# Kernel tuning notes

Hardware: AMD Instinct MI355X
Metric: run time of the kernel (lower is better)

Reference implementation:

```python
import jax, jax.numpy as jnp
import numpy as np

EMB = 512
HEADS = 8


def setup_inputs() -> dict:
    key = jax.random.key(0)
    ks = jax.random.split(key, 9)
    b, t, k, h = 4, 2048, EMB, HEADS
    s = 1.0 / np.sqrt(k)
    x = jax.random.normal(ks[0], (b, t, k), dtype=jnp.float32)
    Wq = jax.random.normal(ks[1], (k, h * k), dtype=jnp.float32) * s
    bq = jnp.zeros((h * k,), dtype=jnp.float32)
    Wk = jax.random.normal(ks[2], (k, h * k), dtype=jnp.float32) * s
    bk = jnp.zeros((h * k,), dtype=jnp.float32)
    Wv = jax.random.normal(ks[3], (k, h * k), dtype=jnp.float32) * s
    bv = jnp.zeros((h * k,), dtype=jnp.float32)
    Wo = jax.random.normal(ks[4], (h * k, k), dtype=jnp.float32) * (1.0 / np.sqrt(h * k))
    bo = jnp.zeros((k,), dtype=jnp.float32)
    return {"x": x, "Wq": Wq, "bq": bq, "Wk": Wk, "bk": bk,
            "Wv": Wv, "bv": bv, "Wo": Wo, "bo": bo}


def reference(x, Wq, bq, Wk, bk, Wv, bv, Wo, bo):
    b, t, k = x.shape
    h = Wq.shape[1] // k
    scale = k ** (-0.25)  # applied to both q and k, matching /= k**(1/4)
    # projections: [b,t,k] -> [b,t,h,k] -> [b,h,t,k]
    q = (x @ Wq + bq).reshape(b, t, h, k).transpose(0, 2, 1, 3) * scale
    kk = (x @ Wk + bk).reshape(b, t, h, k).transpose(0, 2, 1, 3) * scale
    v = (x @ Wv + bv).reshape(b, t, h, k).transpose(0, 2, 1, 3)
    # attention scores [b,h,t,t]
    scores = jnp.einsum('bhqk,bhsk->bhqs', q, kk)
    w = jax.nn.softmax(scores, axis=-1)
    out = jnp.einsum('bhqs,bhsk->bhqk', w, v)  # [b,h,t,k]
    out = out.transpose(0, 2, 1, 3).reshape(b, t, h * k)
    return out @ Wo + bo
```

## Files before the change

### kernel.cpp

```cpp
#include <hip/hip_runtime.h>
#include <hip/hip_bf16.h>
#include <stdint.h>

typedef __hip_bfloat16 bf16;
typedef __bf16 bf16x8 __attribute__((ext_vector_type(8)));
typedef float floatx4 __attribute__((ext_vector_type(4)));

#define AS_LDS __attribute__((address_space(3)))
#define AS_GLB __attribute__((address_space(1)))

__device__ __forceinline__ void gload_lds16(const bf16* g, bf16* l) {
    __builtin_amdgcn_global_load_lds((const AS_GLB void*)g, (AS_LDS void*)l, 16, 0, 0);
}

__global__ void probe_dtype(const float* __restrict__ x, int* __restrict__ flag) {
    __shared__ int cnt;
    if (threadIdx.x == 0) cnt = 0;
    __syncthreads();
    int ok = 0;
    for (int i = threadIdx.x; i < 4096; i += 256) {
        float v = x[i];
        if (v == v && fabsf(v) < 1.0e3f) ok++;
    }
    atomicAdd(&cnt, ok);
    __syncthreads();
    if (threadIdx.x == 0) *flag = (cnt > 2048) ? 1 : 0;
}

__global__ __launch_bounds__(256) void zero_f32(float* __restrict__ p, int n) {
    int i = blockIdx.x * 256 + threadIdx.x;
    if (i < n) p[i] = 0.f;
}

__global__ __launch_bounds__(256) void convert_to_bf16(
    const void* __restrict__ in, bf16* __restrict__ out, long n,
    const int* __restrict__ flag)
{
    long i = ((long)blockIdx.x * 256 + threadIdx.x) * 8;
    if (i >= n) return;
    bf16 o[8];
    if (*flag) {
        const float* p = (const float*)in + i;
        float4 a = *(const float4*)p;
        float4 b = *(const float4*)(p + 4);
        o[0] = __float2bfloat16(a.x); o[1] = __float2bfloat16(a.y);
        o[2] = __float2bfloat16(a.z); o[3] = __float2bfloat16(a.w);
        o[4] = __float2bfloat16(b.x); o[5] = __float2bfloat16(b.y);
        o[6] = __float2bfloat16(b.z); o[7] = __float2bfloat16(b.w);
    } else {
        *(float4*)o = *(const float4*)((const bf16*)in + i);
    }
    *(float4*)&out[i] = *(float4*)o;
}

__global__ __launch_bounds__(256) void emit_out(
    const bf16* __restrict__ in, void* __restrict__ out, long n,
    const int* __restrict__ flag)
{
    long i = ((long)blockIdx.x * 256 + threadIdx.x) * 8;
    if (i >= n) return;
    bf16 v[8];
    *(float4*)v = *(const float4*)&in[i];
    if (*flag) {
        float* o = (float*)out + i;
        float4 a, b;
        a.x = __bfloat162float(v[0]); a.y = __bfloat162float(v[1]);
        a.z = __bfloat162float(v[2]); a.w = __bfloat162float(v[3]);
        b.x = __bfloat162float(v[4]); b.y = __bfloat162float(v[5]);
        b.z = __bfloat162float(v[6]); b.w = __bfloat162float(v[7]);
        *(float4*)o = a;
        *(float4*)(o + 4) = b;
    } else {
        *(float4*)((bf16*)out + i) = *(float4*)v;
    }
}

__global__ __launch_bounds__(256) void transpose_any(
    const void* __restrict__ inv, bf16* __restrict__ out,
    int ldin, int ldout, const int* __restrict__ flag)
{
    __shared__ bf16 tile[64][80];
    const int fp32 = *flag;
    const int c0 = blockIdx.x * 64;
    const int r0 = blockIdx.y * 64;
    const int tid = threadIdx.x;
#pragma unroll
    for (int it = 0; it < 2; ++it) {
        int ch = tid + it * 256;
        int r = ch >> 3, c = (ch & 7) * 8;
        long eidx = (long)(r0 + r) * ldin + (c0 + c);
        if (fp32) {
            const float* p = (const float*)inv + eidx;
            float4 a = *(const float4*)p;
            float4 b = *(const float4*)(p + 4);
            bf16 o[8];
            o[0] = __float2bfloat16(a.x); o[1] = __float2bfloat16(a.y);
            o[2] = __float2bfloat16(a.z); o[3] = __float2bfloat16(a.w);
            o[4] = __float2bfloat16(b.x); o[5] = __float2bfloat16(b.y);
            o[6] = __float2bfloat16(b.z); o[7] = __float2bfloat16(b.w);
            *(float4*)&tile[r][c] = *(float4*)o;
        } else {
            *(float4*)&tile[r][c] = *(const float4*)((const bf16*)inv + eidx);
        }
    }
    __syncthreads();
#pragma unroll
    for (int it = 0; it < 2; ++it) {
        int ch = tid + it * 256;
        int oc = ch >> 3, rb = (ch & 7) * 8;
        bf16 tmp[8];
#pragma unroll
        for (int i = 0; i < 8; ++i) tmp[i] = tile[rb + i][oc];
        *(float4*)&out[(long)(c0 + oc) * ldout + r0 + rb] = *(float4*)tmp;
    }
}

__global__ __launch_bounds__(256) void transpose_bf16(
    const bf16* __restrict__ in, bf16* __restrict__ out,
    int ldin, int ldout,
    int nz1, long in_z1, long out_z1, long in_z2, long out_z2)
{
    __shared__ bf16 tile[64][80];
    const int z = blockIdx.z;
    const int z1 = z % nz1, z2 = z / nz1;
    in  += (long)z1 * in_z1 + (long)z2 * in_z2;
    out += (long)z1 * out_z1 + (long)z2 * out_z2;
    const int c0 = blockIdx.x * 64;
    const int r0 = blockIdx.y * 64;
    const int tid = threadIdx.x;
#pragma unroll
    for (int it = 0; it < 2; ++it) {
        int ch = tid + it * 256;
        int r = ch >> 3, c = (ch & 7) * 8;
        *(float4*)&tile[r][c] = *(const float4*)&in[(long)(r0 + r) * ldin + c0 + c];
    }
    __syncthreads();
#pragma unroll
    for (int it = 0; it < 2; ++it) {
        int ch = tid + it * 256;
        int oc = ch >> 3, rb = (ch & 7) * 8;
        bf16 tmp[8];
#pragma unroll
        for (int i = 0; i < 8; ++i) tmp[i] = tile[rb + i][oc];
        *(float4*)&out[(long)(c0 + oc) * ldout + r0 + rb] = *(float4*)tmp;
    }
}

template <int MODE, int SWZ>
__global__ __launch_bounds__(512, 2) void gemm256(
    const bf16* __restrict__ A, const bf16* __restrict__ Bt,
    bf16* __restrict__ C, const bf16* __restrict__ bias,
    int lda, int ldb, int ldc,
    long az, long bz, long cz, int K, float scale, int qcols,
    bf16* __restrict__ Vt, int vcol0, float* __restrict__ Lsum)
{
    __shared__ bf16 AsL[2][2][256 * 32];
    __shared__ bf16 BsL[2][2][256 * 32];

    const int tid  = threadIdx.x;
    const int lane = tid & 63;
    const int wave = tid >> 6;
    const int wr = wave >> 2;
    const int wc = wave & 3;
    const int lm = lane & 15;
    const int cl = lane >> 4;

    int bxx = blockIdx.x, byy = blockIdx.y, bzz = blockIdx.z;
    if constexpr (SWZ == 1) {
        int flat = bxx + (byy << 3) + (bzz << 6);
        int xcd = flat & 7, idx = flat >> 3;
        bzz = xcd; bxx = idx & 7; byy = idx >> 3;
    } else if constexpr (SWZ == 2) {
        int flat = bxx + byy * 48;
        int xcd = flat & 7, idx = flat >> 3;
        bxx = xcd * 6 + idx % 6; byy = idx / 6; bzz = 0;
    }
    const long zz = bzz;
    A  += zz * az;
    Bt += zz * bz;
    C  += zz * cz;
    float* Lz = (MODE == 1) ? (Lsum + zz * 2048) : nullptr;
    const int m0 = byy * 256;
    const int n0 = bxx * 256;

    int offA[8], offB[4];
#pragma unroll
    for (int i = 0; i < 8; ++i) {
        int row = wr * 128 + i * 16 + lm;
        offA[i] = row * 32 + ((cl ^ ((row >> 1) & 3)) << 3);
    }
#pragma unroll
    for (int j = 0; j < 4; ++j) {
        int row = wc * 64 + j * 16 + lm;
        offB[j] = row * 32 + ((cl ^ ((row >> 1) & 3)) << 3);
    }

    const int sr = lane >> 2;
    const int sc = lane & 3;
    const int NT = K >> 6;

    floatx4 acc[8][4];
#pragma unroll
    for (int i = 0; i < 8; ++i)
#pragma unroll
        for (int j = 0; j < 4; ++j)
            acc[i][j] = (floatx4){0.f, 0.f, 0.f, 0.f};

    auto stageU = [&](int which, int t, int kh) {
        if (t >= NT) return;
        const bf16* G = which ? Bt : A;
        const int ldg  = which ? ldb : lda;
        const int g0   = which ? n0 : m0;
        bf16* lb = which ? &BsL[t & 1][kh][0] : &AsL[t & 1][kh][0];
        const int kcol = t * 64 + kh * 32;
#pragma unroll
        for (int ii = 0; ii < 2; ++ii) {
            int row = ii * 128 + wave * 16 + sr;
            int cg  = sc ^ ((row >> 1) & 3);
            gload_lds16(G + (long)(g0 + row) * ldg + kcol + cg * 8,
                        lb + row * 32 + sc * 8);
        }
    };

    bf16x8 af[8], bfv[2];
    auto dsA = [&](int b, int kh) {
        const bf16* p = &AsL[b][kh][0];
#pragma unroll
        for (int i = 0; i < 8; ++i) af[i] = *(const bf16x8*)(p + offA[i]);
    };
    auto dsB = [&](int b, int kh, int nh) {
        const bf16* p = &BsL[b][kh][0];
        bfv[0] = *(const bf16x8*)(p + offB[nh * 2]);
        bfv[1] = *(const bf16x8*)(p + offB[nh * 2 + 1]);
    };
    auto mfmaQ = [&](int nh) {
        __builtin_amdgcn_s_setprio(1);
#pragma unroll
        for (int i = 0; i < 8; ++i) {
            acc[i][nh * 2] = __builtin_amdgcn_mfma_f32_16x16x32_bf16(
                af[i], bfv[0], acc[i][nh * 2], 0, 0, 0);
            acc[i][nh * 2 + 1] = __builtin_amdgcn_mfma_f32_16x16x32_bf16(
                af[i], bfv[1], acc[i][nh * 2 + 1], 0, 0, 0);
        }
        __builtin_amdgcn_s_setprio(0);
    };

#define BAR    __builtin_amdgcn_s_barrier()
#define SBZ    __builtin_amdgcn_sched_barrier(0)
#define LGKM0  do { asm volatile("s_waitcnt lgkmcnt(0)" ::: "memory"); SBZ; } while (0)
#define VM(n)  do { asm volatile("s_waitcnt vmcnt(" #n ")" ::: "memory"); SBZ; } while (0)

    stageU(0, 0, 0); stageU(1, 0, 0); stageU(0, 0, 1); stageU(1, 0, 1);
    stageU(0, 1, 0); stageU(1, 1, 0);
    VM(4);
    BAR;

    for (int t0 = 0; t0 < NT; t0 += 2) {
        const bool last = (t0 + 2 >= NT);
        dsA(0, 0); dsB(0, 0, 0); stageU(0, t0 + 1, 1);
        BAR; LGKM0; mfmaQ(0); BAR;
        dsB(0, 0, 1); stageU(1, t0 + 1, 1);
        BAR; LGKM0; mfmaQ(1); BAR;
        dsA(0, 1); dsB(0, 1, 0); stageU(0, t0 + 2, 0);
        BAR; LGKM0; mfmaQ(0); BAR;
        dsB(0, 1, 1); stageU(1, t0 + 2, 0);
        BAR; LGKM0; mfmaQ(1);
        if (last) { VM(0); } else { VM(4); }
        BAR;
        dsA(1, 0); dsB(1, 0, 0); stageU(0, t0 + 2, 1);
        BAR; LGKM0; mfmaQ(0); BAR;
        dsB(1, 0, 1); stageU(1, t0 + 2, 1);
        BAR; LGKM0; mfmaQ(1); BAR;
        dsA(1, 1); dsB(1, 1, 0); stageU(0, t0 + 3, 0);
        BAR; LGKM0; mfmaQ(0); BAR;
        dsB(1, 1, 1); stageU(1, t0 + 3, 0);
        BAR; LGKM0; mfmaQ(1);
        if (!last) { VM(4); }
        BAR;
    }
#undef BAR
#undef SBZ
#undef LGKM0
#undef VM

    const int cr = (lane >> 4) * 4;
    if constexpr (MODE == 1) {
#pragma unroll
        for (int j = 0; j < 4; ++j) {
            long q = n0 + wc * 64 + j * 16 + lm;
            bf16* Cr = C + q * ldc + m0 + wr * 128;
            float rs = 0.f;
#pragma unroll
            for (int i = 0; i < 8; ++i) {
                bf16 pk[4];
#pragma unroll
                for (int r = 0; r < 4; ++r) {
                    float e = __expf(acc[i][j][r]);
                    rs += e;
                    pk[r] = __float2bfloat16(e);
                }
                __builtin_nontemporal_store(*(const uint64_t*)pk,
                                            (uint64_t*)&Cr[i * 16 + cr]);
            }
            rs += __shfl_xor(rs, 16);
            rs += __shfl_xor(rs, 32);
            if (cl == 0) atomicAdd(&Lz[q], rs);
        }
    } else {
        if (n0 >= vcol0) {
#pragma unroll
            for (int j = 0; j < 4; ++j) {
                int col = n0 + wc * 64 + j * 16 + lm;
                float bv = __bfloat162float(bias[col]);
                int eg = col - vcol0;
                bf16* vt = Vt + ((long)(eg >> 9) * 512 + (eg & 511)) * 2048;
#pragma unroll
                for (int i = 0; i < 8; ++i) {
                    int t0v = m0 + wr * 128 + i * 16 + cr;
                    bf16 pk[4];
#pragma unroll
                    for (int r = 0; r < 4; ++r)
                        pk[r] = __float2bfloat16(acc[i][j][r] + bv);
                    *(uint64_t*)&vt[t0v] = *(const uint64_t*)pk;
                }
            }
        } else {
            const int l4 = lane & 3;
            float bvj[4], scj[4];
#pragma unroll
            for (int j = 0; j < 4; ++j) {
                int col = n0 + wc * 64 + j * 16 + lm;
                bvj[j] = __bfloat162float(bias[col]);
                scj[j] = (col < qcols) ? scale : 1.0f;
            }
#pragma unroll
            for (int i = 0; i < 8; ++i) {
                int row = m0 + wr * 128 + i * 16 + cr + l4;
                bf16* Cr = C + (long)row * ldc + n0 + wc * 64 + (lm & ~3);
#pragma unroll
                for (int j = 0; j < 4; ++j) {
                    float x0 = (acc[i][j][0] + bvj[j]) * scj[j];
                    float x1 = (acc[i][j][1] + bvj[j]) * scj[j];
                    float x2 = (acc[i][j][2] + bvj[j]) * scj[j];
                    float x3 = (acc[i][j][3] + bvj[j]) * scj[j];
                    float u = __shfl_xor((l4 & 1) ? x0 : x1, 1);
                    float v = __shfl_xor((l4 & 1) ? x2 : x3, 1);
                    if (l4 & 1) { x0 = u; x2 = v; } else { x1 = u; x3 = v; }
                    u = __shfl_xor((l4 & 2) ? x0 : x2, 2);
                    v = __shfl_xor((l4 & 2) ? x1 : x3, 2);
                    if (l4 & 2) { x0 = u; x1 = v; } else { x2 = u; x3 = v; }
                    bf16 pk[4];
                    pk[0] = __float2bfloat16(x0); pk[1] = __float2bfloat16(x1);
                    pk[2] = __float2bfloat16(x2); pk[3] = __float2bfloat16(x3);
                    *(uint64_t*)&Cr[j * 16] = *(const uint64_t*)pk;
                }
            }
        }
    }
}

template <int MODE, int SWZ>
__global__ __launch_bounds__(512, 2) void gemm128n(
    const bf16* __restrict__ A, const bf16* __restrict__ Bt,
    bf16* __restrict__ C, const float* __restrict__ L,
    int lda, int ldb, int ldc,
    long az, long bz, long cz, int K, int kper)
{
    __shared__ bf16 AsL[2][2][128 * 32];
    __shared__ bf16 BsL[2][2][256 * 32];

    const int tid  = threadIdx.x;
    const int lane = tid & 63;
    const int wave = tid >> 6;
    const int wr = wave >> 2;
    const int wc = wave & 3;
    const int lm = lane & 15;
    const int cl = lane >> 4;

    int bxx = blockIdx.x, byy = blockIdx.y, bzz = blockIdx.z;
    if constexpr (SWZ == 5) {
        int flat = bxx + (byy << 3) + (bzz << 5);
        int xcd = flat & 7, idx = flat >> 3;
        bzz = xcd; bxx = idx & 7; byy = idx >> 3;
    } else if constexpr (SWZ == 6) {
        int flat = bxx + (byy << 5) + (bzz << 7);
        int nf = (flat & 7) * 32 + (flat >> 3);
        bzz = nf >> 7; int rr = nf & 127; byy = rr >> 5; bxx = rr & 31;
    }
    const long zz = bzz;
    A  += zz * az;
    Bt += zz * bz;
    C  += zz * cz;
    const float* Lz = (MODE == 5) ? (L + zz * 2048) : nullptr;
    const int kbase = (int)(zz * (long)kper);
    const int m0 = byy * 128;
    const int n0 = bxx * 256;

    int offA[4], offB[4];
#pragma unroll
    for (int i = 0; i < 4; ++i) {
        int row = wr * 64 + i * 16 + lm;
        offA[i] = row * 32 + ((cl ^ ((row >> 1) & 3)) << 3);
    }
#pragma unroll
    for (int j = 0; j < 4; ++j) {
        int row = wc * 64 + j * 16 + lm;
        offB[j] = row * 32 + ((cl ^ ((row >> 1) & 3)) << 3);
    }

    const int sr = lane >> 2;
    const int sc = lane & 3;
    const int NT = K >> 6;

    floatx4 acc[4][4];
#pragma unroll
    for (int i = 0; i < 4; ++i)
#pragma unroll
        for (int j = 0; j < 4; ++j)
            acc[i][j] = (floatx4){0.f, 0.f, 0.f, 0.f};

    auto stageA = [&](int t, int kh) {
        if (t >= NT) return;
        bf16* lb = &AsL[t & 1][kh][0];
        const int kcol = kbase + t * 64 + kh * 32;
        int row = wave * 16 + sr;
        int cg  = sc ^ ((row >> 1) & 3);
        gload_lds16(A + (long)(m0 + row) * lda + kcol + cg * 8,
                    lb + row * 32 + sc * 8);
    };
    auto stageB = [&](int t, int kh) {
        if (t >= NT) return;
        bf16* lb = &BsL[t & 1][kh][0];
        const int kcol = kbase + t * 64 + kh * 32;
#pragma unroll
        for (int ii = 0; ii < 2; ++ii) {
            int row = ii * 128 + wave * 16 + sr;
            int cg  = sc ^ ((row >> 1) & 3);
            gload_lds16(Bt + (long)(n0 + row) * ldb + kcol + cg * 8,
                        lb + row * 32 + sc * 8);
        }
    };

    bf16x8 af[4], bfv[2];
    auto dsA = [&](int b, int kh) {
        const bf16* p = &AsL[b][kh][0];
#pragma unroll
        for (int i = 0; i < 4; ++i) af[i] = *(const bf16x8*)(p + offA[i]);
    };
    auto dsB = [&](int b, int kh, int nh) {
        const bf16* p = &BsL[b][kh][0];
        bfv[0] = *(const bf16x8*)(p + offB[nh * 2]);
        bfv[1] = *(const bf16x8*)(p + offB[nh * 2 + 1]);
    };
    auto mfmaQ = [&](int nh) {
        __builtin_amdgcn_s_setprio(1);
#pragma unroll
        for (int i = 0; i < 4; ++i) {
            acc[i][nh * 2] = __builtin_amdgcn_mfma_f32_16x16x32_bf16(
                af[i], bfv[0], acc[i][nh * 2], 0, 0, 0);
            acc[i][nh * 2 + 1] = __builtin_amdgcn_mfma_f32_16x16x32_bf16(
                af[i], bfv[1], acc[i][nh * 2 + 1], 0, 0, 0);
        }
        __builtin_amdgcn_s_setprio(0);
    };

#define BAR    __builtin_amdgcn_s_barrier()
#define SBZ    __builtin_amdgcn_sched_barrier(0)
#define LGKM0  do { asm volatile("s_waitcnt lgkmcnt(0)" ::: "memory"); SBZ; } while (0)
#define VM(n)  do { asm volatile("s_waitcnt vmcnt(" #n ")" ::: "memory"); SBZ; } while (0)

    stageA(0, 0); stageB(0, 0); stageA(0, 1); stageB(0, 1);
    stageA(1, 0); stageB(1, 0);
    VM(3);
    BAR;

    for (int t0 = 0; t0 < NT; t0 += 2) {
        const bool last = (t0 + 2 >= NT);
        dsA(0, 0); dsB(0, 0, 0); stageA(t0 + 1, 1);
        BAR; LGKM0; mfmaQ(0); BAR;
        dsB(0, 0, 1); stageB(t0 + 1, 1);
        BAR; LGKM0; mfmaQ(1); BAR;
        dsA(0, 1); dsB(0, 1, 0); stageA(t0 + 2, 0);
        BAR; LGKM0; mfmaQ(0); BAR;
        dsB(0, 1, 1); stageB(t0 + 2, 0);
        BAR; LGKM0; mfmaQ(1);
        if (last) { VM(0); } else { VM(3); }
        BAR;
        dsA(1, 0); dsB(1, 0, 0); stageA(t0 + 2, 1);
        BAR; LGKM0; mfmaQ(0); BAR;
        dsB(1, 0, 1); stageB(t0 + 2, 1);
        BAR; LGKM0; mfmaQ(1); BAR;
        dsA(1, 1); dsB(1, 1, 0); stageA(t0 + 3, 0);
        BAR; LGKM0; mfmaQ(0); BAR;
        dsB(1, 1, 1); stageB(t0 + 3, 0);
        BAR; LGKM0; mfmaQ(1);
        if (!last) { VM(3); }
        BAR;
    }
#undef BAR
#undef SBZ
#undef LGKM0
#undef VM

    const int cr = cl * 4;
#pragma unroll
    for (int j = 0; j < 4; ++j) {
        int col = n0 + wc * 64 + j * 16 + lm;
        bf16* Cr = C + (long)col * ldc + m0 + wr * 64;
        float inv = 1.0f;
        if constexpr (MODE == 5) inv = 1.0f / Lz[col];
#pragma unroll
        for (int i = 0; i < 4; ++i) {
            bf16 pk[4];
#pragma unroll
            for (int r = 0; r < 4; ++r)
                pk[r] = __float2bfloat16(acc[i][j][r] * inv);
            *(uint64_t*)&Cr[i * 16 + cr] = *(const uint64_t*)pk;
        }
    }
}

template <int MODE, bool SWAP = false, int SWZ = 0>
__global__ __launch_bounds__(256) void gemm_bt(
    const bf16* __restrict__ A, const bf16* __restrict__ Bt,
    bf16* __restrict__ C, const bf16* __restrict__ bias,
    int lda, int ldb, int ldc,
    long az, long bz, long cz, int K, float scale, int qcols,
    bf16* __restrict__ Vt, int vcol0)
{
    __shared__ bf16 As[128 * 64];
    __shared__ bf16 Bs[128 * 64];

    const int tid  = threadIdx.x;
    const int lane = tid & 63;
    const int wave = tid >> 6;
    const int wx = wave & 1;
    const int wy = wave >> 1;

    int bxx = blockIdx.x, byy = blockIdx.y, bzz = blockIdx.z;
    const long zz = bzz;
    A  += zz * az;
    Bt += zz * bz;
    C  += zz * cz;
    const int bm = SWAP ? bxx : byy;
    const int bn = SWAP ? byy : bxx;
    const int m0 = bm * 128;
    const int n0 = bn * 128;

    const int lm = lane & 15;
    const int kq = (lane >> 4) * 8;

    floatx4 acc[4][4];
#pragma unroll
    for (int i = 0; i < 4; ++i)
#pragma unroll
        for (int j = 0; j < 4; ++j)
            acc[i][j] = (floatx4){0.f, 0.f, 0.f, 0.f};

    for (int kt = 0; kt < K; kt += 64) {
        __syncthreads();
#pragma unroll
        for (int it = 0; it < 4; ++it) {
            int ch = tid + it * 256;
            int r = ch >> 3;
            int c = (ch & 7) * 8;
            gload_lds16(A  + (long)(m0 + r) * lda + (kt + c), &As[ch * 8]);
            gload_lds16(Bt + (long)(n0 + r) * ldb + (kt + c), &Bs[ch * 8]);
        }
        __syncthreads();
#pragma unroll
        for (int kk = 0; kk < 64; kk += 32) {
            bf16x8 af[4], bfv[4];
#pragma unroll
            for (int i = 0; i < 4; ++i)
                af[i] = *(const bf16x8*)&As[(wy * 64 + i * 16 + lm) * 64 + kk + kq];
#pragma unroll
            for (int j = 0; j < 4; ++j)
                bfv[j] = *(const bf16x8*)&Bs[(wx * 64 + j * 16 + lm) * 64 + kk + kq];
#pragma unroll
            for (int i = 0; i < 4; ++i)
#pragma unroll
                for (int j = 0; j < 4; ++j)
                    acc[i][j] = __builtin_amdgcn_mfma_f32_16x16x32_bf16(
                        af[i], bfv[j], acc[i][j], 0, 0, 0);
        }
    }

    const int cr = (lane >> 4) * 4;
    if constexpr (MODE == 1) {
#pragma unroll
        for (int j = 0; j < 4; ++j) {
            int col = n0 + wx * 64 + j * 16 + lm;
#pragma unroll
            for (int i = 0; i < 4; ++i)
#pragma unroll
                for (int r = 0; r < 4; ++r) {
                    int row = m0 + wy * 64 + i * 16 + cr + r;
                    C[(long)row * ldc + col] = __float2bfloat16(__expf(acc[i][j][r]));
                }
        }
    } else {
#pragma unroll
        for (int j = 0; j < 4; ++j) {
            int col = n0 + wx * 64 + j * 16 + lm;
            float bv = (MODE == 0 && bias) ? __bfloat162float(bias[col]) : 0.f;
            float sc = (col < qcols) ? scale : 1.0f;
#pragma unroll
            for (int i = 0; i < 4; ++i) {
#pragma unroll
                for (int r = 0; r < 4; ++r) {
                    int row = m0 + wy * 64 + i * 16 + cr + r;
                    long idx = (long)row * ldc + col;
                    float v;
                    if (MODE == 2) v = acc[i][j][r] + __bfloat162float(C[idx]);
                    else           v = (acc[i][j][r] + bv) * sc;
                    C[idx] = __float2bfloat16(v);
                }
            }
        }
    }
}

template <bool SWAP = false>
__global__ __launch_bounds__(256) void gemm_bt_splitk(
    const bf16* __restrict__ A, const bf16* __restrict__ Bt,
    bf16* __restrict__ P, int lda, int ldb, int ldp,
    long az, long bz, long pz, long skStride, int nsk, int Kc)
{
    __shared__ bf16 As[128 * 64];
    __shared__ bf16 Bs[128 * 64];

    const int tid  = threadIdx.x;
    const int lane = tid & 63;
    const int wave = tid >> 6;
    const int wx = wave & 1;
    const int wy = wave >> 1;
    const int zz = blockIdx.z;
    const int ks = zz % nsk;
    const int zh = zz / nsk;
    A  += (long)zh * az;
    Bt += (long)zh * bz;
    bf16* Pz = P + (long)zh * pz + (long)ks * skStride;
    const int bm = SWAP ? blockIdx.x : blockIdx.y;
    const int bn = SWAP ? blockIdx.y : blockIdx.x;
    const int m0 = bm * 128;
    const int n0 = bn * 128;
    const int k0 = ks * Kc;

    const int lm = lane & 15;
    const int kq = (lane >> 4) * 8;

    floatx4 acc[4][4];
#pragma unroll
    for (int i = 0; i < 4; ++i)
#pragma unroll
        for (int j = 0; j < 4; ++j)
            acc[i][j] = (floatx4){0.f, 0.f, 0.f, 0.f};

    for (int kt = k0; kt < k0 + Kc; kt += 64) {
        __syncthreads();
#pragma unroll
        for (int it = 0; it < 4; ++it) {
            int ch = tid + it * 256;
            int r = ch >> 3;
            int c = (ch & 7) * 8;
            gload_lds16(A  + (long)(m0 + r) * lda + (kt + c), &As[ch * 8]);
            gload_lds16(Bt + (long)(n0 + r) * ldb + (kt + c), &Bs[ch * 8]);
        }
        __syncthreads();
#pragma unroll
        for (int kk = 0; kk < 64; kk += 32) {
            bf16x8 af[4], bfv[4];
#pragma unroll
            for (int i = 0; i < 4; ++i)
                af[i] = *(const bf16x8*)&As[(wy * 64 + i * 16 + lm) * 64 + kk + kq];
#pragma unroll
            for (int j = 0; j < 4; ++j)
                bfv[j] = *(const bf16x8*)&Bs[(wx * 64 + j * 16 + lm) * 64 + kk + kq];
#pragma unroll
            for (int i = 0; i < 4; ++i)
#pragma unroll
                for (int j = 0; j < 4; ++j)
                    acc[i][j] = __builtin_amdgcn_mfma_f32_16x16x32_bf16(
                        af[i], bfv[j], acc[i][j], 0, 0, 0);
        }
    }

    const int cr = (lane >> 4) * 4;
#pragma unroll
    for (int j = 0; j < 4; ++j) {
        int col = n0 + wx * 64 + j * 16 + lm;
#pragma unroll
        for (int i = 0; i < 4; ++i)
#pragma unroll
            for (int r = 0; r < 4; ++r) {
                int row = m0 + wy * 64 + i * 16 + cr + r;
                Pz[(long)row * ldp + col] = __float2bfloat16(acc[i][j][r]);
            }
    }
}

__global__ __launch_bounds__(256) void reduce_emit(
    const bf16* __restrict__ P, const bf16* __restrict__ bias,
    void* __restrict__ out, long MN, int N,
    const int* __restrict__ flag)
{
    long i = ((long)blockIdx.x * 256 + threadIdx.x) * 8;
    if (i >= MN) return;
    bf16 bb[8], a[8], b[8];
    *(float4*)bb = *(const float4*)&bias[i & (N - 1)];
    *(float4*)a  = *(const float4*)&P[i];
    *(float4*)b  = *(const float4*)&P[MN + i];
    float s[8];
#pragma unroll
    for (int k = 0; k < 8; ++k)
        s[k] = __bfloat162float(bb[k]) + __bfloat162float(a[k]) + __bfloat162float(b[k]);
    if (*flag) {
        float* o = (float*)out + i;
        float4 lo = {s[0], s[1], s[2], s[3]};
        float4 hi = {s[4], s[5], s[6], s[7]};
        *(float4*)o = lo;
        *(float4*)(o + 4) = hi;
    } else {
        bf16 o[8];
#pragma unroll
        for (int k = 0; k < 8; ++k) o[k] = __float2bfloat16(s[k]);
        *(float4*)&((bf16*)out)[i] = *(float4*)o;
    }
}

__global__ __launch_bounds__(256) void reduce_splitk(
    const bf16* __restrict__ P, const bf16* __restrict__ bias,
    bf16* __restrict__ Out, long MN, int N, int SK)
{
    long i = ((long)blockIdx.x * 256 + threadIdx.x) * 8;
    if (i >= MN) return;
    float s[8];
    if (bias) {
        bf16 bb[8];
        *(float4*)bb = *(const float4*)&bias[i & (N - 1)];
#pragma unroll
        for (int k = 0; k < 8; ++k) s[k] = __bfloat162float(bb[k]);
    } else {
#pragma unroll
        for (int k = 0; k < 8; ++k) s[k] = 0.f;
    }
    for (int z = 0; z < SK; ++z) {
        bf16 a[8];
        *(float4*)a = *(const float4*)&P[(long)z * MN + i];
#pragma unroll
        for (int k = 0; k < 8; ++k) s[k] += __bfloat162float(a[k]);
    }
    bf16 o[8];
#pragma unroll
    for (int k = 0; k < 8; ++k) o[k] = __float2bfloat16(s[k]);
    *(float4*)&Out[i] = *(float4*)o;
}

__global__ __launch_bounds__(256) void softmax_rows2048(bf16* __restrict__ S)
{
    __shared__ float red[8];
    const long row = blockIdx.x;
    bf16* p = S + row * 2048;
    const int tid = threadIdx.x;
    float4 raw = *(const float4*)&p[tid * 8];
    bf16 vb[8];
    *(float4*)vb = raw;
    float v[8];
#pragma unroll
    for (int i = 0; i < 8; ++i) v[i] = __bfloat162float(vb[i]);
    float m = v[0];
#pragma unroll
    for (int i = 1; i < 8; ++i) m = fmaxf(m, v[i]);
#pragma unroll
    for (int o = 32; o > 0; o >>= 1) m = fmaxf(m, __shfl_xor(m, o));
    if ((tid & 63) == 0) red[tid >> 6] = m;
    __syncthreads();
    m = fmaxf(fmaxf(red[0], red[1]), fmaxf(red[2], red[3]));
    float s = 0.f;
#pragma unroll
    for (int i = 0; i < 8; ++i) { v[i] = __expf(v[i] - m); s += v[i]; }
#pragma unroll
    for (int o = 32; o > 0; o >>= 1) s += __shfl_xor(s, o);
    if ((tid & 63) == 0) red[4 + (tid >> 6)] = s;
    __syncthreads();
    s = (red[4] + red[5]) + (red[6] + red[7]);
    float inv = 1.f / s;
#pragma unroll
    for (int i = 0; i < 8; ++i) vb[i] = __float2bfloat16(v[i] * inv);
    *(float4*)&p[tid * 8] = *(float4*)vb;
}

extern "C" void kernel_launch(void* const* d_in, const int* in_sizes, int n_in,
                              void* d_out, int out_size, void* d_ws, size_t ws_size,
                              hipStream_t stream)
{
    const int Bb = 4, T = 2048, E = 512, H = 8;
    const int HE = H * E;
    const int N3 = 3 * HE;
    const int N2 = 2 * HE;
    const int M  = Bb * T;
    const long NX = (long)M * E;

    const void* xr = nullptr;
    const void* Wr[4] = {nullptr, nullptr, nullptr, nullptr};
    const void* br[3] = {nullptr, nullptr, nullptr};
    const void* bor = nullptr;
    int nw = 0, nb = 0;
    for (int i = 0; i < n_in; ++i) {
        int s = in_sizes[i];
        if      (s == (int)NX)      xr = d_in[i];
        else if (s == E * HE)       { if (nw < 4) Wr[nw++] = d_in[i]; }
        else if (s == HE)           { if (nb < 3) br[nb++] = d_in[i]; }
        else if (s == E)            bor = d_in[i];
    }
    if (!xr || nw < 4 || nb < 3 || !bor) {
        xr = d_in[0]; Wr[0] = d_in[1]; br[0] = d_in[2]; Wr[1] = d_in[3];
        br[1] = d_in[4]; Wr[2] = d_in[5]; br[2] = d_in[6]; Wr[3] = d_in[7];
        bor = d_in[8];
    }

    const float qscale = 0.04419417382415922f;
    const int   QC = 1 << 30;
    dim3 blk(256);

    bf16* pool = (bf16*)d_ws;
    int*  flag = (int*)(void*)pool;
    bf16* xc   = pool + 8;
    bf16* bqc  = xc  + NX;
    bf16* bkc  = bqc + HE;
    bf16* bvc  = bkc + HE;
    bf16* boc  = bvc + HE;
    bf16* WqT  = boc + E;
    const size_t w2m = (size_t)E * HE;
    bf16* WkT  = WqT + w2m;
    bf16* WvT  = WkT + w2m;
    bf16* WoT  = WvT + w2m;
    bf16* Ofin = WoT + w2m;
    bf16* p0   = Ofin + NX;

    const size_t wsE    = ws_size / sizeof(bf16);
    const size_t fixedE = (size_t)(p0 - pool);
    const size_t wQK   = (size_t)T * N2;
    const size_t wQKV  = (size_t)T * N3;
    const size_t wBat  = (size_t)T * HE;
    const size_t wHd   = (size_t)T * E;
    const size_t sAll  = (size_t)H * T * T;
    const size_t sOne  = (size_t)T * T;
    const size_t wBig  = (size_t)M * HE;
    const size_t wL    = 32768;
    const size_t needB2 = fixedE + wQK + wBat + sAll + wBig + wL;
    const size_t needB  = fixedE + wQKV + 2 * wBat + sAll;
    const size_t needC  = fixedE + 5 * wBat + sOne;
    const size_t needD  = fixedE + 5 * wHd  + sOne;
    if (wsE < needD) return;

    probe_dtype<<<dim3(1), blk, 0, stream>>>((const float*)xr, flag);
    convert_to_bf16<<<dim3((unsigned)((NX / 8 + 255) / 256)), blk, 0, stream>>>(
        xr, xc, NX, flag);
    convert_to_bf16<<<dim3(2), blk, 0, stream>>>(br[0], bqc, HE, flag);
    convert_to_bf16<<<dim3(2), blk, 0, stream>>>(br[1], bkc, HE, flag);
    convert_to_bf16<<<dim3(2), blk, 0, stream>>>(br[2], bvc, HE, flag);
    convert_to_bf16<<<dim3(1), blk, 0, stream>>>(bor, boc, E, flag);
    transpose_any<<<dim3(HE / 64, E / 64, 1), blk, 0, stream>>>(Wr[0], WqT, HE, E, flag);
    transpose_any<<<dim3(HE / 64, E / 64, 1), blk, 0, stream>>>(Wr[1], WkT, HE, E, flag);
    transpose_any<<<dim3(HE / 64, E / 64, 1), blk, 0, stream>>>(Wr[2], WvT, HE, E, flag);
    transpose_any<<<dim3(E / 64, HE / 64, 1), blk, 0, stream>>>(Wr[3], WoT, E, HE, flag);

    if (wsE >= needB2) {
        bf16* QKb = p0;
        bf16* Vtb = QKb + wQK;
        bf16* S   = Vtb + wBat;
        bf16* Oatt = S + sAll;
        float* Lbuf = (float*)(Oatt + wBig);

        for (int b = 0; b < Bb; ++b) {
            const bf16* xb = xc + (size_t)b * T * E;
            gemm256<4, 2><<<dim3(N3 / 256, T / 256, 1), dim3(512), 0, stream>>>(
                xb, WqT, QKb, bqc, E, E, N2, 0, 0, 0, E, qscale, HE, Vtb, N2,
                nullptr);
            zero_f32<<<dim3(64), blk, 0, stream>>>(Lbuf, H * T);
            gemm256<1, 1><<<dim3(T / 256, T / 256, H), dim3(512), 0, stream>>>(
                QKb + HE, QKb, S, nullptr, N2, N2, T,
                (long)E, (long)E, (long)T * T, E, 1.f, QC, nullptr, 0, Lbuf);
            gemm128n<5, 5><<<dim3(T / 256, E / 128, H), dim3(512), 0, stream>>>(
                Vtb, S, Oatt + (size_t)b * T * HE, Lbuf, T, T, HE,
                (long)E * T, (long)T * T, (long)E, T, 0);
        }
        gemm128n<6, 6><<<dim3(M / 256, E / 128, 2), dim3(512), 0, stream>>>(
            WoT, Oatt, QKb, nullptr, HE, HE, E,
            0, 0, (long)M * E, HE / 2, HE / 2);
        reduce_emit<<<dim3((unsigned)((NX / 8 + 255) / 256)), blk, 0, stream>>>(
            QKb, boc, d_out, NX, E, flag);
        return;
    }

    if (wsE >= needB) {
        bf16* QKVb = p0;
        bf16* Vtb  = QKVb + wQKV;
        bf16* Oatt = Vtb + wBat;
        bf16* S    = Oatt + wBat;

        for (int b = 0; b < Bb; ++b) {
            const bf16* xb = xc + (size_t)b * T * E;
            gemm_bt<0><<<dim3(N3 / 128, T / 128, 1), blk, 0, stream>>>(
                xb, WqT, QKVb, bqc, E, E, N3, 0, 0, 0, E, qscale, HE, nullptr, 0);
            transpose_bf16<<<dim3(E / 64, T / 64, H), blk, 0, stream>>>(
                QKVb + 2 * HE, Vtb, N3, T, H, (long)E, (long)E * T, 0, 0);
            gemm_bt<0><<<dim3(T / 128, T / 128, H), blk, 0, stream>>>(
                QKVb, QKVb + HE, S, nullptr, N3, N3, T,
                (long)E, (long)E, (long)T * T, E, 1.f, QC, nullptr, 0);
            softmax_rows2048<<<dim3(H * T, 1, 1), blk, 0, stream>>>(S);
            gemm_bt<0><<<dim3(E / 128, T / 128, H), blk, 0, stream>>>(
                S, Vtb, Oatt, nullptr, T, T, HE,
                (long)T * T, (long)E * T, (long)E, T, 1.f, QC, nullptr, 0);
            gemm_bt_splitk<false><<<dim3(E / 128, T / 128, 8), blk, 0, stream>>>(
                Oatt, WoT, (bf16*)S, HE, HE, E, 0, 0, 0, (long)T * E, 8, HE / 8);
            reduce_splitk<<<dim3((unsigned)(((long)T * E / 8 + 255) / 256)), blk, 0, stream>>>(
                (bf16*)S, boc, Ofin + (size_t)b * T * E, (long)T * E, E, 8);
        }
    } else if (wsE >= needC) {
        bf16* Qb  = p0;
        bf16* Kb  = Qb  + wBat;
        bf16* Vb  = Kb  + wBat;
        bf16* Vtb = Vb  + wBat;
        bf16* Ob  = Vtb + wBat;
        bf16* S   = Ob  + wBat;

        for (int b = 0; b < Bb; ++b) {
            const bf16* xb = xc + (size_t)b * T * E;
            gemm_bt<0><<<dim3(HE / 128, T / 128, 1), blk, 0, stream>>>(
                xb, WqT, Qb, bqc, E, E, HE, 0, 0, 0, E, qscale, QC, nullptr, 0);
            gemm_bt<0><<<dim3(HE / 128, T / 128, 1), blk, 0, stream>>>(
                xb, WkT, Kb, bkc, E, E, HE, 0, 0, 0, E, 1.f, QC, nullptr, 0);
            gemm_bt<0><<<dim3(HE / 128, T / 128, 1), blk, 0, stream>>>(
                xb, WvT, Vb, bvc, E, E, HE, 0, 0, 0, E, 1.f, QC, nullptr, 0);
            transpose_bf16<<<dim3(E / 64, T / 64, H), blk, 0, stream>>>(
                Vb, Vtb, HE, T, H, (long)E, (long)E * T, 0, 0);
            for (int h = 0; h < H; ++h) {
                gemm_bt<0><<<dim3(T / 128, T / 128, 1), blk, 0, stream>>>(
                    Qb + (size_t)h * E, Kb + (size_t)h * E, S, nullptr,
                    HE, HE, T, 0, 0, 0, E, 1.f, QC, nullptr, 0);
                softmax_rows2048<<<dim3(T, 1, 1), blk, 0, stream>>>(S);
                gemm_bt<0><<<dim3(E / 128, T / 128, 1), blk, 0, stream>>>(
                    S, Vtb + (size_t)h * E * T, Ob + (size_t)h * E, nullptr,
                    T, T, HE, 0, 0, 0, T, 1.f, QC, nullptr, 0);
            }
            gemm_bt<0><<<dim3(E / 128, T / 128, 1), blk, 0, stream>>>(
                Ob, WoT, Ofin + (size_t)b * T * E, boc,
                HE, HE, E, 0, 0, 0, HE, 1.f, QC, nullptr, 0);
        }
    } else {
        bf16* Qh  = p0;
        bf16* Kh  = Qh  + wHd;
        bf16* Vh  = Kh  + wHd;
        bf16* Vth = Vh  + wHd;
        bf16* Oh  = Vth + wHd;
        bf16* S   = Oh  + wHd;

        for (int b = 0; b < Bb; ++b) {
            const bf16* xb = xc + (size_t)b * T * E;
            bf16* outb = Ofin + (size_t)b * T * E;
            for (int h = 0; h < H; ++h) {
                const size_t hw = (size_t)h * E * E;
                gemm_bt<0><<<dim3(E / 128, T / 128, 1), blk, 0, stream>>>(
                    xb, WqT + hw, Qh, bqc + (size_t)h * E, E, E, E,
                    0, 0, 0, E, qscale, QC, nullptr, 0);
                gemm_bt<0><<<dim3(E / 128, T / 128, 1), blk, 0, stream>>>(
                    xb, WkT + hw, Kh, bkc + (size_t)h * E, E, E, E,
                    0, 0, 0, E, 1.f, QC, nullptr, 0);
                gemm_bt<0><<<dim3(E / 128, T / 128, 1), blk, 0, stream>>>(
                    xb, WvT + hw, Vh, bvc + (size_t)h * E, E, E, E,
                    0, 0, 0, E, 1.f, QC, nullptr, 0);
                transpose_bf16<<<dim3(E / 64, T / 64, 1), blk, 0, stream>>>(
                    Vh, Vth, E, T, 1, 0, 0, 0, 0);
                gemm_bt<0><<<dim3(T / 128, T / 128, 1), blk, 0, stream>>>(
                    Qh, Kh, S, nullptr, E, E, T, 0, 0, 0, E, 1.f, QC, nullptr, 0);
                softmax_rows2048<<<dim3(T, 1, 1), blk, 0, stream>>>(S);
                gemm_bt<0><<<dim3(E / 128, T / 128, 1), blk, 0, stream>>>(
                    S, Vth, Oh, nullptr, T, T, E, 0, 0, 0, T, 1.f, QC, nullptr, 0);
                if (h == 0)
                    gemm_bt<0><<<dim3(E / 128, T / 128, 1), blk, 0, stream>>>(
                        Oh, WoT, outb, boc, E, HE, E, 0, 0, 0, E, 1.f, QC, nullptr, 0);
                else
                    gemm_bt<2><<<dim3(E / 128, T / 128, 1), blk, 0, stream>>>(
                        Oh, WoT + (size_t)h * E, outb, nullptr,
                        E, HE, E, 0, 0, 0, E, 1.f, QC, nullptr, 0);
            }
        }
    }

    emit_out<<<dim3((unsigned)((NX / 8 + 255) / 256)), blk, 0, stream>>>(
        Ofin, d_out, NX, flag);
}
```

Baseline: 892.9 us.

## Add dedicated P·V GEMM kernel with full-width V tiles and head-interleaved grid

Replaces the generic gemm128n P·V launch with a new gemm_pv kernel. Each block covers all 512 V-embedding rows against a 64-query tile, so every score tile is read once instead of once per 128-row embedding chunk. The grid is remapped so consecutive blocks cycle across heads, and the 1/L normalisation is applied in the epilogue. The exp-score store in the QK kernel also switches from a nontemporal store to a normal store, likely so S stays in cache for the following kernel. The larger A tile uses more LDS and registers per block, which may reduce occupancy.

```diff
diff --git a/kernel.cpp b/kernel.cpp
--- a/kernel.cpp
+++ b/kernel.cpp
@@ -299,8 +299,7 @@
                     rs += e;
                     pk[r] = __float2bfloat16(e);
                 }
-                __builtin_nontemporal_store(*(const uint64_t*)pk,
-                                            (uint64_t*)&Cr[i * 16 + cr]);
+                *(uint64_t*)&Cr[i * 16 + cr] = *(const uint64_t*)pk;
             }
             rs += __shfl_xor(rs, 16);
             rs += __shfl_xor(rs, 32);
@@ -355,6 +354,148 @@
                     *(uint64_t*)&Cr[j * 16] = *(const uint64_t*)pk;
                 }
             }
+        }
+    }
+}
+
+__global__ __launch_bounds__(512, 2) void gemm_pv(
+    const bf16* __restrict__ A, const bf16* __restrict__ Bt,
+    bf16* __restrict__ C, const float* __restrict__ L,
+    int lda, int ldb, int ldc, long az, long bz, long cz, int K)
+{
+    __shared__ bf16 AsL[2][2][512 * 32];
+    __shared__ bf16 BsL[2][64 * 64];
+
+    const int tid  = threadIdx.x;
+    const int lane = tid & 63;
+    const int wave = tid >> 6;
+    const int wm = wave >> 1;
+    const int wn = wave & 1;
+    const int lm = lane & 15;
+    const int cl = lane >> 4;
+
+    int flat = blockIdx.x + (blockIdx.z << 5);
+    const long zz = flat & 7;
+    const int qt = flat >> 3;
+    A  += zz * az;
+    Bt += zz * bz;
+    C  += zz * cz;
+    const float* Lz = L + zz * 2048;
+    const int n0 = qt * 64;
+
+    int offA[8];
+#pragma unroll
+    for (int i = 0; i < 8; ++i) {
+        int row = wm * 128 + i * 16 + lm;
+        offA[i] = row * 32 + ((cl ^ ((row >> 1) & 3)) << 3);
+    }
+    int rB[2], gB0[2];
+#pragma unroll
+    for (int j = 0; j < 2; ++j) {
+        rB[j] = wn * 32 + j * 16 + lm;
+        gB0[j] = rB[j] & 7;
+    }
+
+    const int sr = lane >> 2;
+    const int sc = lane & 3;
+    const int NT = K >> 6;
+
+    floatx4 acc[8][2];
+#pragma unroll
+    for (int i = 0; i < 8; ++i)
+#pragma unroll
+        for (int j = 0; j < 2; ++j)
+            acc[i][j] = (floatx4){0.f, 0.f, 0.f, 0.f};
+
+    auto stageA = [&](int t, int kh) {
+        if (t >= NT) return;
+        bf16* lb = &AsL[t & 1][kh][0];
+        const int kcol = t * 64 + kh * 32;
+#pragma unroll
+        for (int seg = 0; seg < 4; ++seg) {
+            int row = seg * 128 + wave * 16 + sr;
+            int cg  = sc ^ ((row >> 1) & 3);
+            gload_lds16(A + (long)row * lda + kcol + cg * 8,
+                        lb + row * 32 + sc * 8);
+        }
+    };
+    auto stageB = [&](int t) {
+        if (t >= NT) return;
+        bf16* lb = &BsL[t & 1][0];
+        const int kcol = t * 64;
+        int row = wave * 8 + (lane >> 3);
+        int cg  = (lane & 7) ^ (row & 7);
+        gload_lds16(Bt + (long)(n0 + row) * ldb + kcol + cg * 8,
+                    lb + row * 64 + (lane & 7) * 8);
+    };
+
+    bf16x8 af[8], bfv[2];
+    auto dsA = [&](int b, int kh) {
+        const bf16* p = &AsL[b][kh][0];
+#pragma unroll
+        for (int i = 0; i < 8; ++i) af[i] = *(const bf16x8*)(p + offA[i]);
+    };
+    auto dsB = [&](int b, int kh) {
+        const bf16* p = &BsL[b][0];
+#pragma unroll
+        for (int j = 0; j < 2; ++j) {
+            int g = (kh * 4 + cl) ^ gB0[j];
+            bfv[j] = *(const bf16x8*)(p + rB[j] * 64 + g * 8);
+        }
+    };
+    auto mfmaQ = [&]() {
+        __builtin_amdgcn_s_setprio(1);
+#pragma unroll
+        for (int i = 0; i < 8; ++i) {
+            acc[i][0] = __builtin_amdgcn_mfma_f32_16x16x32_bf16(
+                af[i], bfv[0], acc[i][0], 0, 0, 0);
+            acc[i][1] = __builtin_amdgcn_mfma_f32_16x16x32_bf16(
+                af[i], bfv[1], acc[i][1], 0, 0, 0);
+        }
+        __builtin_amdgcn_s_setprio(0);
+    };
+
+#define BAR    __builtin_amdgcn_s_barrier()
+#define SBZ    __builtin_amdgcn_sched_barrier(0)
+#define LGKM0  do { asm volatile("s_waitcnt lgkmcnt(0)" ::: "memory"); SBZ; } while (0)
+#define VM(n)  do { asm volatile("s_waitcnt vmcnt(" #n ")" ::: "memory"); SBZ; } while (0)
+
+    stageA(0, 0); stageB(0); stageA(0, 1); stageA(1, 0);
+    VM(4);
+    BAR;
+
+    for (int t0 = 0; t0 < NT; t0 += 2) {
+        const bool last = (t0 + 2 >= NT);
+        dsA(0, 0); dsB(0, 0); stageA(t0 + 1, 1); stageB(t0 + 1);
+        BAR; LGKM0; mfmaQ(); BAR;
+        dsA(0, 1); dsB(0, 1); stageA(t0 + 2, 0);
+        BAR; LGKM0; mfmaQ();
+        if (last) { VM(0); } else { VM(4); }
+        BAR;
+        dsA(1, 0); dsB(1, 0); stageA(t0 + 2, 1); stageB(t0 + 2);
+        BAR; LGKM0; mfmaQ(); BAR;
+        dsA(1, 1); dsB(1, 1); stageA(t0 + 3, 0);
+        BAR; LGKM0; mfmaQ();
+        if (!last) { VM(4); }
+        BAR;
+    }
+#undef BAR
+#undef SBZ
+#undef LGKM0
+#undef VM
+
+#pragma unroll
+    for (int j = 0; j < 2; ++j) {
+        int col = n0 + wn * 32 + j * 16 + lm;
+        float inv = 1.0f / Lz[col];
+        bf16* Cr = C + (long)col * ldc + wm * 128;
+#pragma unroll
+        for (int i = 0; i < 8; ++i) {
+            bf16 pk[4];
+#pragma unroll
+            for (int r = 0; r < 4; ++r)
+                pk[r] = __float2bfloat16(acc[i][j][r] * inv);
+            *(uint64_t*)&Cr[i * 16 + cl * 4] = *(const uint64_t*)pk;
         }
     }
 }
@@ -883,9 +1024,9 @@
             gemm256<1, 1><<<dim3(T / 256, T / 256, H), dim3(512), 0, stream>>>(
                 QKb + HE, QKb, S, nullptr, N2, N2, T,
                 (long)E, (long)E, (long)T * T, E, 1.f, QC, nullptr, 0, Lbuf);
-            gemm128n<5, 5><<<dim3(T / 256, E / 128, H), dim3(512), 0, stream>>>(
+            gemm_pv<<<dim3(T / 64, 1, H), dim3(512), 0, stream>>>(
                 Vtb, S, Oatt + (size_t)b * T * HE, Lbuf, T, T, HE,
-                (long)E * T, (long)T * T, (long)E, T, 0);
+                (long)E * T, (long)T * T, (long)E, T);
         }
         gemm128n<6, 6><<<dim3(M / 256, E / 128, 2), dim3(512), 0, stream>>>(
             WoT, Oatt, QKb, nullptr, HE, HE, E,
```

After: 981.0 us. 9.9% more time.
